# Kernel tuning notes

Measured on AMD Instinct MI355X. Metric: run time of the kernel, lower is better.

The kernel has to match this reference:

```python
import jax, jax.numpy as jnp
import numpy as np

EPS = 1e-8

def _cdist(a, b):
    # Euclidean pairwise distances, torch.cdist(p=2) equivalent.
    sq = (jnp.sum(a * a, axis=1)[:, None] + jnp.sum(b * b, axis=1)[None, :]
          - 2.0 * (a @ b.T))
    return jnp.sqrt(jnp.maximum(sq, 1e-12))

def setup_inputs() -> dict:
    key = jax.random.key(0)
    k1, k2, k3, k4, k5, k6 = jax.random.split(key, 6)
    ns, n_cls, n_feat, K = 4096, 500, 256, 400
    return {
        "src_x": jax.random.normal(k1, (ns, n_feat), dtype=jnp.float32),
        "tgt_x": jax.random.normal(k2, (ns, n_feat), dtype=jnp.float32),
        "src_y": jax.random.uniform(k3, (ns, n_cls), dtype=jnp.float32),
        "tgt_y": jax.random.uniform(k4, (ns, n_cls), dtype=jnp.float32),
        "queue": jax.random.normal(k5, (n_cls, n_feat, K), dtype=jnp.float32),
        "queue_size": jax.random.randint(k6, (n_cls,), 0, K, dtype=jnp.int32),
    }

def reference(src_x, tgt_x, src_y, tgt_y, queue, queue_size):
    n_cls, n_feat, K = queue.shape
    num = queue_size.astype(queue.dtype)[:, None]                      # (C,1)
    # src_centroid: masked mean over the first queue_size[c] columns
    valid = (jnp.arange(K)[None, :] < queue_size[:, None]).astype(queue.dtype)  # (C,K)
    centroid = jnp.einsum('cfk,ck->cf', queue, valid) / jnp.maximum(num, 1.0)
    centroid = jnp.where(num > 0, centroid, 0.0)                       # (C,F)

    batch_src = src_y.T @ src_x                                        # (C,F)
    total_num = num + jnp.sum(src_y, axis=0)[:, None] + EPS            # (C,1)
    mean_src = (centroid * num + batch_src) / total_num                # (C,F)

    batch_prob = jnp.sum(tgt_y, axis=0)[:, None] + EPS                 # (C,1)
    mean_tgt = (tgt_y.T @ tgt_x) / batch_prob                          # (C,F)

    intra = jnp.diagonal(_cdist(mean_src, mean_tgt)).mean()
    inter = _cdist(mean_src, mean_src).mean()
    return intra, inter
```

## Files before the change

kernel.cpp:

```cpp
#include <hip/hip_runtime.h>
#include <math.h>

#define NS 4096
#define NC 500
#define NF 256
#define NK 400
#define KC_GEMM 16
#define KC_CS   32

#define NB_GEMM (32 * KC_GEMM * 2)
#define NB_CS   (KC_CS * 2)
#define NB_QUE  ((NC * NF) / 4)

__global__ __launch_bounds__(256) void k_heavy(
    const float* __restrict__ Xs, const float* __restrict__ Ys, float* __restrict__ Ps,
    const float* __restrict__ Xt, const float* __restrict__ Yt, float* __restrict__ Pt,
    float* __restrict__ CSs, float* __restrict__ CSt,
    const float* __restrict__ queue, const int* __restrict__ qsize,
    float* __restrict__ qsum) {
  __shared__ float ytile[NS / KC_GEMM][16];
  const int bid = blockIdx.x;

  if (bid < NB_GEMM) {
    const int z   = bid >> 9;
    const int rem = bid & 511;
    const int kc  = rem >> 5;
    const int c0  = (rem & 31) * 16;
    const float* X = z ? Xt : Xs;
    const float* Y = z ? Yt : Ys;
    float*       P = z ? Pt : Ps;
    const int n0   = kc * (NS / KC_GEMM);
    const int cmax = (NC - c0 < 16) ? (NC - c0) : 16;

    for (int i = threadIdx.x; i < (NS / KC_GEMM) * 16; i += 256) {
      int r = i >> 4, cc = i & 15;
      ytile[r][cc] = (cc < cmax) ? Y[(size_t)(n0 + r) * NC + c0 + cc] : 0.f;
    }
    __syncthreads();

    const int f = threadIdx.x;
    float acc[16];
    #pragma unroll
    for (int j = 0; j < 16; ++j) acc[j] = 0.f;

    #pragma unroll 4
    for (int n = 0; n < NS / KC_GEMM; ++n) {
      float xv = X[(size_t)(n0 + n) * NF + f];
      #pragma unroll
      for (int j = 0; j < 16; ++j) acc[j] = fmaf(ytile[n][j], xv, acc[j]);
    }
    #pragma unroll
    for (int j = 0; j < 16; ++j)
      if (c0 + j < NC) P[((size_t)kc * NC + c0 + j) * NF + f] = acc[j];

  } else if (bid < NB_GEMM + NB_CS) {
    const int b = bid - NB_GEMM;
    const float* Y = (b >> 5) ? Yt : Ys;
    float*      CS = (b >> 5) ? CSt : CSs;
    const int kc = b & 31;
    const int n0 = kc * (NS / KC_CS);
    const int t  = threadIdx.x;
    float s0 = 0.f, s1 = 0.f;
    for (int n = n0; n < n0 + NS / KC_CS; ++n) {
      const float* row = Y + (size_t)n * NC;
      s0 += row[t];
      if (t + 256 < NC) s1 += row[t + 256];
    }
    CS[kc * 512 + t] = s0;
    if (t + 256 < NC) CS[kc * 512 + t + 256] = s1;

  } else {
    const int qb   = bid - (NB_GEMM + NB_CS);
    const int wave = qb * 4 + (threadIdx.x >> 6);
    const int lane = threadIdx.x & 63;
    const int c    = wave >> 8;
    const int qs   = qsize[c];
    const float* base = queue + (size_t)wave * NK;
    float s = 0.f;
    {
      int k = 4 * lane;
      float4 v = *reinterpret_cast<const float4*>(base + k);
      if (k + 0 < qs) s += v.x;
      if (k + 1 < qs) s += v.y;
      if (k + 2 < qs) s += v.z;
      if (k + 3 < qs) s += v.w;
    }
    if (lane < 36) {
      int k = 256 + 4 * lane;
      float4 v = *reinterpret_cast<const float4*>(base + k);
      if (k + 0 < qs) s += v.x;
      if (k + 1 < qs) s += v.y;
      if (k + 2 < qs) s += v.z;
      if (k + 3 < qs) s += v.w;
    }
    #pragma unroll
    for (int m = 32; m; m >>= 1) s += __shfl_xor(s, m);
    if (lane == 0) qsum[wave] = s;
  }
}

__global__ __launch_bounds__(256) void k_means(
    const float* __restrict__ qsum, const int* __restrict__ qsize,
    const float* __restrict__ Psrc, const float* __restrict__ Ptgt,
    const float* __restrict__ CSsrc, const float* __restrict__ CStgt,
    float* __restrict__ MS, float* __restrict__ MT, float* __restrict__ ipart) {
  const int c = blockIdx.x, f = threadIdx.x;
  float cs_s = 0.f, cs_t = 0.f;
  #pragma unroll
  for (int kc = 0; kc < KC_CS; ++kc) {
    cs_s += CSsrc[kc * 512 + c];
    cs_t += CStgt[kc * 512 + c];
  }
  float num = (float)qsize[c];
  float ns = qsum[(size_t)c * NF + f];
  float nt = 0.f;
  #pragma unroll
  for (int kc = 0; kc < KC_GEMM; ++kc) {
    ns += Psrc[((size_t)kc * NC + c) * NF + f];
    nt += Ptgt[((size_t)kc * NC + c) * NF + f];
  }
  float ms = ns / (num + cs_s + 1e-8f);
  float mt = nt / (cs_t + 1e-8f);
  MS[(size_t)c * NF + f] = ms;
  MT[(size_t)c * NF + f] = mt;

  float d = ms - mt;
  float s = d * d;
  #pragma unroll
  for (int m = 32; m; m >>= 1) s += __shfl_xor(s, m);
  __shared__ float red[4];
  int wid = f >> 6, lane = f & 63;
  if (lane == 0) red[wid] = s;
  __syncthreads();
  if (f == 0) ipart[c] = sqrtf(fmaxf(red[0] + red[1] + red[2] + red[3], 1e-12f));
}

#define TC 16
#define NBT 32
__global__ __launch_bounds__(256) void k_dist(const float* __restrict__ MS,
                                              float* __restrict__ epart) {
  __shared__ float a[TC][NF + 4];
  __shared__ float b[TC][NF + 4];
  const int bi = blockIdx.x & (NBT - 1);
  const int bj = blockIdx.x >> 5;

  for (int i = threadIdx.x; i < TC * (NF / 4); i += 256) {
    int r = i >> 6, fq = (i & 63) * 4;
    int c1 = bi * TC + r;
    int c2 = bj * TC + r;
    float4 va = (c1 < NC) ? *reinterpret_cast<const float4*>(&MS[(size_t)c1 * NF + fq])
                          : make_float4(0.f, 0.f, 0.f, 0.f);
    float4 vb = (c2 < NC) ? *reinterpret_cast<const float4*>(&MS[(size_t)c2 * NF + fq])
                          : make_float4(0.f, 0.f, 0.f, 0.f);
    *reinterpret_cast<float4*>(&a[r][fq]) = va;
    *reinterpret_cast<float4*>(&b[r][fq]) = vb;
  }
  __syncthreads();

  const int i1 = threadIdx.x >> 4, i2 = threadIdx.x & 15;
  float s = 0.f;
  #pragma unroll 8
  for (int fq = 0; fq < NF; fq += 4) {
    float4 va = *reinterpret_cast<const float4*>(&a[i1][fq]);
    float4 vb = *reinterpret_cast<const float4*>(&b[i2][fq]);
    float d0 = va.x - vb.x, d1 = va.y - vb.y, d2 = va.z - vb.z, d3 = va.w - vb.w;
    s = fmaf(d0, d0, s); s = fmaf(d1, d1, s); s = fmaf(d2, d2, s); s = fmaf(d3, d3, s);
  }
  bool valid = (bi * TC + i1 < NC) && (bj * TC + i2 < NC);
  float r = valid ? sqrtf(fmaxf(s, 1e-12f)) : 0.f;

  #pragma unroll
  for (int m = 32; m; m >>= 1) r += __shfl_xor(r, m);
  __shared__ float red[4];
  int wid = threadIdx.x >> 6, lane = threadIdx.x & 63;
  if (lane == 0) red[wid] = r;
  __syncthreads();
  if (threadIdx.x == 0) epart[blockIdx.x] = red[0] + red[1] + red[2] + red[3];
}

__global__ __launch_bounds__(1024) void k_final(const float* __restrict__ ipart,
                                                const float* __restrict__ epart,
                                                float* __restrict__ out) {
  const int t = threadIdx.x;
  float si = (t < NC) ? ipart[t] : 0.f;
  float se = epart[t];
  #pragma unroll
  for (int m = 32; m; m >>= 1) { si += __shfl_xor(si, m); se += __shfl_xor(se, m); }
  __shared__ float ri[16], re[16];
  int wid = t >> 6, lane = t & 63;
  if (lane == 0) { ri[wid] = si; re[wid] = se; }
  __syncthreads();
  if (t == 0) {
    float A = 0.f, B = 0.f;
    #pragma unroll
    for (int w = 0; w < 16; ++w) { A += ri[w]; B += re[w]; }
    out[0] = A / (float)NC;
    out[1] = B / ((float)NC * (float)NC);
  }
}

extern "C" void kernel_launch(void* const* d_in, const int* in_sizes, int n_in,
                              void* d_out, int out_size, void* d_ws, size_t ws_size,
                              hipStream_t stream) {
  const float* src_x = (const float*)d_in[0];
  const float* tgt_x = (const float*)d_in[1];
  const float* src_y = (const float*)d_in[2];
  const float* tgt_y = (const float*)d_in[3];
  const float* queue = (const float*)d_in[4];
  const int*   qsize = (const int*)d_in[5];
  float* out = (float*)d_out;

  float* ws    = (float*)d_ws;
  float* qsum  = ws;
  float* Psrc  = qsum + NC * NF;
  float* Ptgt  = Psrc + (size_t)KC_GEMM * NC * NF;
  float* CSs   = Ptgt + (size_t)KC_GEMM * NC * NF;
  float* CSt   = CSs + KC_CS * 512;
  float* MS    = CSt + KC_CS * 512;
  float* MT    = MS + NC * NF;
  float* ipart = MT + NC * NF;
  float* epart = ipart + NC;

  k_heavy<<<NB_GEMM + NB_CS + NB_QUE, 256, 0, stream>>>(
      src_x, src_y, Psrc, tgt_x, tgt_y, Ptgt, CSs, CSt, queue, qsize, qsum);

  k_means<<<NC, 256, 0, stream>>>(qsum, qsize, Psrc, Ptgt, CSs, CSt, MS, MT, ipart);

  k_dist<<<NBT * NBT, 256, 0, stream>>>(MS, epart);

  k_final<<<1, 1024, 0, stream>>>(ipart, epart, out);
}
```

Before: 91.46 us.

## Register-tile the Y^T X partial GEMM and skip queue loads past queue_size

The partial GEMM is rewritten so each block covers 64 classes by 256 features. X and Y chunks are staged in shared memory with float4 loads, and each thread accumulates an 8x8 outer-product tile. This cuts redundant X reads across class tiles and gives each shared load more FMAs. The partial buffers are padded to 512 classes for aligned vector stores. The queue reduction now only loads float4 chunks that fall within queue_size, which removes memory traffic on the largest input in exchange for lane divergence.

```diff
diff --git a/kernel.cpp b/kernel.cpp
--- a/kernel.cpp
+++ b/kernel.cpp
@@ -3,12 +3,16 @@
 
 #define NS 4096
 #define NC 500
+#define NCP 512
 #define NF 256
 #define NK 400
 #define KC_GEMM 16
 #define KC_CS   32
-
-#define NB_GEMM (32 * KC_GEMM * 2)
+#define CT 64
+#define NCT 8
+#define NN 16
+
+#define NB_GEMM (NCT * KC_GEMM * 2)
 #define NB_CS   (KC_CS * 2)
 #define NB_QUE  ((NC * NF) / 4)
 
@@ -18,40 +22,74 @@
     float* __restrict__ CSs, float* __restrict__ CSt,
     const float* __restrict__ queue, const int* __restrict__ qsize,
     float* __restrict__ qsum) {
-  __shared__ float ytile[NS / KC_GEMM][16];
+  __shared__ float yA[NN][32], yB[NN][32];
+  __shared__ float xA[NN][128], xB[NN][128];
   const int bid = blockIdx.x;
 
   if (bid < NB_GEMM) {
-    const int z   = bid >> 9;
-    const int rem = bid & 511;
-    const int kc  = rem >> 5;
-    const int c0  = (rem & 31) * 16;
+    const int z   = bid >> 7;
+    const int rem = bid & 127;
+    const int kc  = rem >> 3;
+    const int ct  = rem & 7;
     const float* X = z ? Xt : Xs;
     const float* Y = z ? Yt : Ys;
     float*       P = z ? Pt : Ps;
-    const int n0   = kc * (NS / KC_GEMM);
-    const int cmax = (NC - c0 < 16) ? (NC - c0) : 16;
-
-    for (int i = threadIdx.x; i < (NS / KC_GEMM) * 16; i += 256) {
-      int r = i >> 4, cc = i & 15;
-      ytile[r][cc] = (cc < cmax) ? Y[(size_t)(n0 + r) * NC + c0 + cc] : 0.f;
-    }
-    __syncthreads();
-
-    const int f = threadIdx.x;
-    float acc[16];
-    #pragma unroll
-    for (int j = 0; j < 16; ++j) acc[j] = 0.f;
-
-    #pragma unroll 4
-    for (int n = 0; n < NS / KC_GEMM; ++n) {
-      float xv = X[(size_t)(n0 + n) * NF + f];
+    const int c0 = ct * CT;
+    const int n0 = kc * (NS / KC_GEMM);
+    const int tid = threadIdx.x;
+    const int fg = tid & 31;
+    const int cg = tid >> 5;
+
+    float acc[8][8];
+    #pragma unroll
+    for (int j = 0; j < 8; ++j)
       #pragma unroll
-      for (int j = 0; j < 16; ++j) acc[j] = fmaf(ytile[n][j], xv, acc[j]);
-    }
-    #pragma unroll
-    for (int j = 0; j < 16; ++j)
-      if (c0 + j < NC) P[((size_t)kc * NC + c0 + j) * NF + f] = acc[j];
+      for (int k = 0; k < 8; ++k) acc[j][k] = 0.f;
+
+    for (int nn0 = 0; nn0 < NS / KC_GEMM; nn0 += NN) {
+      {
+        int r = tid >> 4, q = tid & 15;
+        int c = c0 + q * 4;
+        float4 v = (c < NC) ? *reinterpret_cast<const float4*>(&Y[(size_t)(n0 + nn0 + r) * NC + c])
+                            : make_float4(0.f, 0.f, 0.f, 0.f);
+        float* dst = (q & 1) ? &yB[r][(q >> 1) * 4] : &yA[r][(q >> 1) * 4];
+        *reinterpret_cast<float4*>(dst) = v;
+      }
+      #pragma unroll
+      for (int t = 0; t < 4; ++t) {
+        int idx = tid + 256 * t;
+        int r = idx >> 6, q = idx & 63;
+        float4 v = *reinterpret_cast<const float4*>(&X[(size_t)(n0 + nn0 + r) * NF + q * 4]);
+        float* dst = (q & 1) ? &xB[r][(q >> 1) * 4] : &xA[r][(q >> 1) * 4];
+        *reinterpret_cast<float4*>(dst) = v;
+      }
+      __syncthreads();
+
+      #pragma unroll 4
+      for (int r = 0; r < NN; ++r) {
+        float4 y0 = *reinterpret_cast<float4*>(&yA[r][cg * 4]);
+        float4 y1 = *reinterpret_cast<float4*>(&yB[r][cg * 4]);
+        float4 x0 = *reinterpret_cast<float4*>(&xA[r][fg * 4]);
+        float4 x1 = *reinterpret_cast<float4*>(&xB[r][fg * 4]);
+        float yv[8] = {y0.x, y0.y, y0.z, y0.w, y1.x, y1.y, y1.z, y1.w};
+        float xv[8] = {x0.x, x0.y, x0.z, x0.w, x1.x, x1.y, x1.z, x1.w};
+        #pragma unroll
+        for (int j = 0; j < 8; ++j)
+          #pragma unroll
+          for (int k = 0; k < 8; ++k)
+            acc[j][k] = fmaf(yv[j], xv[k], acc[j][k]);
+      }
+      __syncthreads();
+    }
+    #pragma unroll
+    for (int j = 0; j < 8; ++j) {
+      int c = c0 + cg * 8 + j;
+      if (c < NC) {
+        float* dst = &P[((size_t)kc * NCP + c) * NF + fg * 8];
+        *reinterpret_cast<float4*>(dst)     = make_float4(acc[j][0], acc[j][1], acc[j][2], acc[j][3]);
+        *reinterpret_cast<float4*>(dst + 4) = make_float4(acc[j][4], acc[j][5], acc[j][6], acc[j][7]);
+      }
+    }
 
   } else if (bid < NB_GEMM + NB_CS) {
     const int b = bid - NB_GEMM;
@@ -75,20 +113,21 @@
     const int lane = threadIdx.x & 63;
     const int c    = wave >> 8;
     const int qs   = qsize[c];
+    const int L    = (qs + 3) >> 2;
     const float* base = queue + (size_t)wave * NK;
     float s = 0.f;
-    {
+    if (lane < L) {
       int k = 4 * lane;
       float4 v = *reinterpret_cast<const float4*>(base + k);
-      if (k + 0 < qs) s += v.x;
+      s += v.x;
       if (k + 1 < qs) s += v.y;
       if (k + 2 < qs) s += v.z;
       if (k + 3 < qs) s += v.w;
     }
-    if (lane < 36) {
+    if (lane + 64 < L) {
       int k = 256 + 4 * lane;
       float4 v = *reinterpret_cast<const float4*>(base + k);
-      if (k + 0 < qs) s += v.x;
+      s += v.x;
       if (k + 1 < qs) s += v.y;
       if (k + 2 < qs) s += v.z;
       if (k + 3 < qs) s += v.w;
@@ -116,8 +155,8 @@
   float nt = 0.f;
   #pragma unroll
   for (int kc = 0; kc < KC_GEMM; ++kc) {
-    ns += Psrc[((size_t)kc * NC + c) * NF + f];
-    nt += Ptgt[((size_t)kc * NC + c) * NF + f];
+    ns += Psrc[((size_t)kc * NCP + c) * NF + f];
+    nt += Ptgt[((size_t)kc * NCP + c) * NF + f];
   }
   float ms = ns / (num + cs_s + 1e-8f);
   float mt = nt / (cs_t + 1e-8f);
@@ -213,8 +252,8 @@
   float* ws    = (float*)d_ws;
   float* qsum  = ws;
   float* Psrc  = qsum + NC * NF;
-  float* Ptgt  = Psrc + (size_t)KC_GEMM * NC * NF;
-  float* CSs   = Ptgt + (size_t)KC_GEMM * NC * NF;
+  float* Ptgt  = Psrc + (size_t)KC_GEMM * NCP * NF;
+  float* CSs   = Ptgt + (size_t)KC_GEMM * NCP * NF;
   float* CSt   = CSs + KC_CS * 512;
   float* MS    = CSt + KC_CS * 512;
   float* MT    = MS + NC * NF;
```

New measurement: 112.5 us. 23.0% more time.
